# Optimization experiments

Measured on AMD Instinct MI355X. Metric: run time of the kernel, lower is better.

Reference implementation:

```python
import jax, jax.numpy as jnp
import numpy as np

SCALE_BASE = 512.0
GN_EPS = 1e-5


def _xpos(x, downscale):
    # x: [..., L, D]; XPOS rotary embedding with exponential length scale (torchscale)
    L, D = x.shape[-2], x.shape[-1]
    half = D // 2
    base = (jnp.arange(0, D, 2, dtype=jnp.float32) + 0.4 * D) / (1.4 * D)  # [half]
    min_pos = -(L // 2)
    power = (jnp.arange(min_pos, min_pos + L, dtype=jnp.float32) / SCALE_BASE)[:, None]
    scale = base[None, :] ** power  # [L, half]
    inv_freq = 1.0 / (10000.0 ** (jnp.arange(half, dtype=jnp.float32) / half))
    ang = jnp.arange(L, dtype=jnp.float32)[:, None] * inv_freq[None, :]  # [L, half]
    sin, cos = jnp.sin(ang), jnp.cos(ang)
    if downscale:
        scale = 1.0 / scale
    sin_s = jnp.repeat(sin * scale, 2, axis=-1)  # duplicate_interleave -> [L, D]
    cos_s = jnp.repeat(cos * scale, 2, axis=-1)
    x1, x2 = x[..., ::2], x[..., 1::2]
    rot = jnp.stack((-x2, x1), axis=-1).reshape(x.shape)  # rotate_every_two
    return x * cos_s + rot * sin_s


def _decay_mask(L, H):
    gammas = 1.0 - jnp.exp(jnp.linspace(np.log(1.0 / 32.0), np.log(1.0 / 512.0), H)).astype(jnp.float32)
    idx = jnp.arange(L)
    dist = idx[:, None] - idx[None, :]  # [L, L]
    causal = dist >= 0
    d = jnp.maximum(dist, 0).astype(jnp.float32)
    # gamma^|n-s| below diagonal, 0 above (gamma^inf = 0 in the torch version)
    return jnp.where(causal[None], gammas[:, None, None] ** d[None], 0.0)  # [H, L, L]


def setup_inputs() -> dict:
    key = jax.random.key(0)
    ks = jax.random.split(key, 9)
    B, L, D, H = 2, 2048, 1024, 16
    hd = D // H
    return {
        "query": jax.random.normal(ks[0], (B, L, D), jnp.float32),
        "key": jax.random.normal(ks[1], (B, L, D), jnp.float32),
        "value": jax.random.normal(ks[2], (B, L, D), jnp.float32),
        "W_Q": jax.random.normal(ks[3], (H, D, hd), jnp.float32) / D,
        "W_K": jax.random.normal(ks[4], (H, D, hd), jnp.float32) / D,
        "W_V": jax.random.normal(ks[5], (H, D, hd), jnp.float32) / D,
        "g_w": jax.random.normal(ks[6], (D, D), jnp.float32) * (2.0 / (D + D)) ** 0.5,
        "g_b": jnp.zeros((D,), jnp.float32),
        "out_w": jax.random.normal(ks[7], (D, D), jnp.float32) * (2.0 / (D + D)) ** 0.5,
        "out_b": jnp.zeros((D,), jnp.float32),
    }


def reference(query, key, value, W_Q, W_K, W_V, g_w, g_b, out_w, out_b):
    B, L, D = query.shape
    H = W_Q.shape[0]
    q = jnp.einsum('bld,hde->bhle', query, W_Q)
    k = jnp.einsum('bld,hde->bhle', key, W_K)
    v = jnp.einsum('bld,hde->bhle', value, W_V)
    q = _xpos(q, downscale=False)
    k = _xpos(k, downscale=True)
    # retention_parallel: QK^T * decay mask (no softmax, no scale), then @ V
    sim = jnp.einsum('bhnd,bhsd->bhns', q, k) * _decay_mask(L, H)[None]
    ret = jnp.einsum('bhns,bhsd->bhnd', sim, v)  # [B, H, L, hd]
    # GroupNorm(num_groups=H, affine=False) on (b n, h d): normalize per (b, h, n) over hd
    mu = ret.mean(axis=-1, keepdims=True)
    var = ret.var(axis=-1, keepdims=True)
    ret = (ret - mu) / jnp.sqrt(var + GN_EPS)
    ret = ret.transpose(0, 2, 1, 3).reshape(B, L, D)  # b h n d -> b n (h d)
    gate = jax.nn.silu(query @ g_w.T + g_b)
    return (ret * gate) @ out_w.T + out_b
```

## Files before the change

kernel.cpp:

```cpp
#include <hip/hip_runtime.h>
#include <cstdint>

#define B_  2
#define L_  2048
#define D_  1024
#define H_  16
#define HD_ 64
#define M_  (B_*L_)

#define MD  4194304u
#define DD  1048576u

#define OFF_XQB  0u
#define OFF_XKB  (MD)
#define OFF_XVB  (2u*MD)
#define OFF_WQT  (3u*MD)
#define OFF_WKT  (3u*MD + DD)
#define OFF_WVT  (3u*MD + 2u*DD)
#define OFF_GWB  (3u*MD + 3u*DD)
#define OFF_OWB  (3u*MD + 4u*DD)
#define OFF_GATE (3u*MD + 5u*DD)
#define OFF_QB2  (OFF_GATE + MD)
#define OFF_KB2  (OFF_QB2 + MD)
#define OFF_VTG  (OFF_KB2 + MD)
#define OFF_ABUF (OFF_VTG + MD)
#define OFF_F32  (OFF_ABUF + MD)

typedef __attribute__((ext_vector_type(8))) short bf16x8;
typedef __attribute__((ext_vector_type(4))) short s16x4;
typedef __attribute__((ext_vector_type(4))) float f32x4;

__device__ __forceinline__ unsigned short f2b(float x){
  union { float f; unsigned u; } a; a.f = x;
  unsigned r = a.u + 0x7FFFu + ((a.u >> 16) & 1u);
  return (unsigned short)(r >> 16);
}
__device__ __forceinline__ float b2f(unsigned short u){
  union { unsigned u; float f; } a; a.u = ((unsigned)u) << 16; return a.f;
}

__global__ __launch_bounds__(256) void prep_kernel(
    const float* __restrict__ q, const float* __restrict__ k,
    const float* __restrict__ v, const float* __restrict__ gw,
    const float* __restrict__ ow, const float* __restrict__ WQ,
    const float* __restrict__ WK, const float* __restrict__ WV,
    unsigned short* __restrict__ ws)
{
  __shared__ float t[32][33];
  const int bx = blockIdx.x, tid = threadIdx.x;
  if (bx < 14336) {
    size_t i = ((size_t)bx * 256 + tid) * 4;
    const float* src; unsigned short* dst;
    if (i < MD)            { src = q  + i;              dst = ws + OFF_XQB + i; }
    else if (i < 2u*MD)    { src = k  + (i - MD);       dst = ws + OFF_XKB + (i - MD); }
    else if (i < 3u*MD)    { src = v  + (i - 2u*MD);    dst = ws + OFF_XVB + (i - 2u*MD); }
    else if (i < 3u*MD+DD) { src = gw + (i - 3u*MD);    dst = ws + OFF_GWB + (i - 3u*MD); }
    else                   { src = ow + (i - 3u*MD-DD); dst = ws + OFF_OWB + (i - 3u*MD - DD); }
    float4 vv = *(const float4*)src;
    ushort4 o; o.x = f2b(vv.x); o.y = f2b(vv.y); o.z = f2b(vv.z); o.w = f2b(vv.w);
    *(ushort4*)dst = o;
  } else if (bx < 17408) {
    const int tb = bx - 14336;
    const int w = tb >> 10;
    const int tb2 = tb & 1023;
    const int h = tb2 >> 6, tt = tb2 & 63;
    const int e0 = (tt & 1) * 32, d0 = (tt >> 1) * 32;
    const float* in = (w == 0) ? WQ : (w == 1) ? WK : WV;
    unsigned short* out = ws + ((w == 0) ? OFF_WQT : (w == 1) ? OFF_WKT : OFF_WVT);
    const int x = tid & 31, y0 = tid >> 5;
    for (int yy = y0; yy < 32; yy += 8)
      t[yy][x] = in[((size_t)h * D_ + d0 + yy) * HD_ + e0 + x];
    __syncthreads();
    for (int yy = y0; yy < 32; yy += 8)
      out[((size_t)h * HD_ + e0 + yy) * D_ + d0 + x] = f2b(t[x][yy]);
  } else {
    float* fb = (float*)(ws + OFF_F32);
    const int idx = (bx - 17408) * 256 + tid;
    const int l = idx >> 5, i = idx & 31;
    const float base = (2.0f * (float)i + 0.4f * (float)HD_) / (1.4f * (float)HD_);
    const float p = (float)(l - L_ / 2) * (1.0f / 512.0f);
    const float sc = exp2f(p * log2f(base));
    const float invf = exp2f(-(float)i * (13.287712379549449f / 32.0f));
    float s, c; sincosf((float)l * invf, &s, &c);
    fb[          l * 32 + i] = c * sc;
    fb[ 65536 +  l * 32 + i] = s * sc;
    const float is = 1.0f / sc;
    fb[131072 +  l * 32 + i] = c * is;
    fb[196608 +  l * 32 + i] = s * is;
  }
}

__device__ __forceinline__ void gemm_body(
    const unsigned short* __restrict__ A, const unsigned short* __restrict__ Bt,
    float* __restrict__ outF, unsigned short* __restrict__ outB,
    const float* __restrict__ ct, const float* __restrict__ st,
    const float* __restrict__ bias, int mode, int ldc, int M0, int N0,
    char* As, char* Bs)
{
  const int tid = threadIdx.x;
  const int wave = tid >> 6, lane = tid & 63;
  const int wm = wave & 1, wn = wave >> 1;
  const int mlane = lane & 15, kgrp = lane >> 4;
  const int rl = lane >> 3, csel = lane & 7;
  const char* Ab = (const char*)A;
  const char* Bb = (const char*)Bt;

  f32x4 acc[4][2] = {};

  for (int K0 = 0; K0 < 1024; K0 += 64) {
    __syncthreads();
#pragma unroll
    for (int t = 0; t < 4; ++t) {
      const int row = wave * 32 + t * 8 + rl;
      const int gc = csel ^ (row & 7);
      const char* ga = Ab + ((size_t)(M0 + row) * 1024 + K0) * 2 + gc * 16;
      __builtin_amdgcn_global_load_lds(
          (const __attribute__((address_space(1))) void*)ga,
          (__attribute__((address_space(3))) void*)(As + (wave * 32 + t * 8) * 128 + lane * 16),
          16, 0, 0);
    }
#pragma unroll
    for (int t = 0; t < 2; ++t) {
      const int row = wave * 16 + t * 8 + rl;
      const int gc = csel ^ (row & 7);
      const char* gb = Bb + ((size_t)(N0 + row) * 1024 + K0) * 2 + gc * 16;
      __builtin_amdgcn_global_load_lds(
          (const __attribute__((address_space(1))) void*)gb,
          (__attribute__((address_space(3))) void*)(Bs + (wave * 16 + t * 8) * 128 + lane * 16),
          16, 0, 0);
    }
    __syncthreads();
#pragma unroll
    for (int kh = 0; kh < 2; ++kh) {
      bf16x8 af[4], bfr[2];
#pragma unroll
      for (int tm = 0; tm < 4; ++tm) {
        const int r = wm * 64 + tm * 16 + mlane;
        af[tm] = *(const bf16x8*)(As + r * 128 + (((kh * 4 + kgrp) ^ (r & 7)) << 4));
      }
#pragma unroll
      for (int tn = 0; tn < 2; ++tn) {
        const int r = wn * 32 + tn * 16 + mlane;
        bfr[tn] = *(const bf16x8*)(Bs + r * 128 + (((kh * 4 + kgrp) ^ (r & 7)) << 4));
      }
#pragma unroll
      for (int tm = 0; tm < 4; ++tm)
#pragma unroll
        for (int tn = 0; tn < 2; ++tn)
          acc[tm][tn] = __builtin_amdgcn_mfma_f32_16x16x32_bf16(af[tm], bfr[tn], acc[tm][tn], 0, 0, 0);
    }
  }

#pragma unroll
  for (int tm = 0; tm < 4; ++tm)
#pragma unroll
    for (int tn = 0; tn < 2; ++tn) {
      f32x4 v = acc[tm][tn];
#pragma unroll
      for (int r = 0; r < 4; ++r) {
        const int grow = M0 + wm * 64 + tm * 16 + (lane >> 4) * 4 + r;
        const int gcol = N0 + wn * 32 + tn * 16 + mlane;
        float val = v[r];
        if (mode == 1 || mode == 2) {
          const float partner = __shfl_xor(val, 1);
          const int l = grow & (L_ - 1);
          const int i = (gcol >> 1) & 31;
          const float c = ct[l * 32 + i], s = st[l * 32 + i];
          val = (gcol & 1) ? (val * c + partner * s) : (val * c - partner * s);
          outB[(size_t)grow * ldc + gcol] = f2b(val);
        } else if (mode == 0) {
          outB[(size_t)grow * ldc + gcol] = f2b(val);
        } else if (mode == 3) {
          const float x = val + bias[gcol];
          outB[(size_t)grow * ldc + gcol] = f2b(x / (1.0f + expf(-x)));
        } else {
          outF[(size_t)grow * ldc + gcol] = val + bias[gcol];
        }
      }
    }
}

__global__ __launch_bounds__(256) void gemm4_kernel(
    unsigned short* __restrict__ ws, const float* __restrict__ g_b)
{
  __shared__ __align__(16) char As[128 * 128];
  __shared__ __align__(16) char Bs[64 * 128];
  const int z = blockIdx.y, bx = blockIdx.x;
  float* fb = (float*)(ws + OFF_F32);
  const unsigned short *A, *Bt; unsigned short* outB;
  const float *ct = nullptr, *st = nullptr, *bias = nullptr;
  int mode, ldc, M0, N0;
  if (z == 0) {
    A = ws + OFF_XQB; Bt = ws + OFF_WQT; outB = ws + OFF_QB2;
    ct = fb; st = fb + 65536; mode = 1; ldc = D_;
    M0 = (bx & 31) * 128; N0 = (bx >> 5) * 64;
  } else if (z == 1) {
    A = ws + OFF_XKB; Bt = ws + OFF_WKT; outB = ws + OFF_KB2;
    ct = fb + 131072; st = fb + 196608; mode = 2; ldc = D_;
    M0 = (bx & 31) * 128; N0 = (bx >> 5) * 64;
  } else if (z == 2) {
    A = ws + OFF_WVT; Bt = ws + OFF_XVB; outB = ws + OFF_VTG;
    mode = 0; ldc = M_;
    M0 = (bx & 7) * 128; N0 = (bx >> 3) * 64;
  } else {
    A = ws + OFF_XQB; Bt = ws + OFF_GWB; outB = ws + OFF_GATE;
    bias = g_b; mode = 3; ldc = D_;
    M0 = (bx & 31) * 128; N0 = (bx >> 5) * 64;
  }
  gemm_body(A, Bt, nullptr, outB, ct, st, bias, mode, ldc, M0, N0, As, Bs);
}

__global__ __launch_bounds__(256) void gemm_final_kernel(
    unsigned short* __restrict__ ws, const float* __restrict__ out_b,
    float* __restrict__ out)
{
  __shared__ __align__(16) char As[128 * 128];
  __shared__ __align__(16) char Bs[64 * 128];
  gemm_body(ws + OFF_ABUF, ws + OFF_OWB, out, nullptr, nullptr, nullptr,
            out_b, 4, D_, blockIdx.x * 128, blockIdx.y * 64, As, Bs);
}

#define AQ_OFF 0
#define AK_OFF 8192
#define AV_OFF 16384
#define AP_OFF 24576

__global__ __launch_bounds__(256) void attn_mfma_kernel(
    const unsigned short* __restrict__ qg, const unsigned short* __restrict__ kg,
    const unsigned short* __restrict__ vtg, const unsigned short* __restrict__ gate,
    unsigned short* __restrict__ Abuf)
{
  __shared__ __align__(16) char smem[32768];
  const int tid = threadIdx.x, wave = tid >> 6, lane = tid & 63;
  const int mlane = lane & 15, kgrp = lane >> 4;
  const int rl = lane >> 3, csel = lane & 7;

  const int id = blockIdx.x;
  const int bh = id & 31, p = id >> 5;
  const int b = bh >> 4, h = bh & 15;

  const float lo   = -3.4657359027997265f;
  const float step = -0.1848392481493187f;
  const float gamma = 1.0f - expf(lo + (float)h * step);
  const float lg2g  = log2f(gamma);
  const float g1    = exp2f(-lg2g);
  const float gmr[4] = {1.0f, g1, g1 * g1, g1 * g1 * g1};

#pragma unroll 1
  for (int half = 0; half < 2; ++half) {
    const int xq = half ? (31 - p) : p;
    const int l0 = xq * 64;

    __syncthreads();
#pragma unroll
    for (int t = 0; t < 2; ++t) {
      const int row = 16 * wave + 8 * t + rl;
      const char* g = (const char*)(qg + (size_t)(b * L_ + l0 + row) * D_ + h * HD_ + ((csel ^ (row & 7)) << 3));
      __builtin_amdgcn_global_load_lds(
          (const __attribute__((address_space(1))) void*)g,
          (__attribute__((address_space(3))) void*)(smem + AQ_OFF + (16 * wave + 8 * t) * 128 + lane * 16),
          16, 0, 0);
    }
    __syncthreads();

    bf16x8 qa[2];
    {
      const int row = 16 * wave + mlane;
#pragma unroll
      for (int kk = 0; kk < 2; ++kk)
        qa[kk] = *(const bf16x8*)(smem + AQ_OFF + row * 128 + (((4 * kk + kgrp) ^ (row & 7)) << 4));
    }
    const float rqm = exp2f((float)(l0 + 16 * wave + mlane) * lg2g);

    f32x4 racc[4] = {};

    for (int it = 0; it <= xq; ++it) {
      const int s0 = it * 64;
      __syncthreads();
#pragma unroll
      for (int t = 0; t < 2; ++t) {
        const int row = 16 * wave + 8 * t + rl;
        const char* gk = (const char*)(kg + (size_t)(b * L_ + s0 + row) * D_ + h * HD_ + ((csel ^ (row & 7)) << 3));
        __builtin_amdgcn_global_load_lds(
            (const __attribute__((address_space(1))) void*)gk,
            (__attribute__((address_space(3))) void*)(smem + AK_OFF + (16 * wave + 8 * t) * 128 + lane * 16),
            16, 0, 0);
        const char* gv = (const char*)(vtg + (size_t)(h * HD_ + row) * M_ + b * L_ + s0 + ((csel ^ (row & 7)) << 3));
        __builtin_amdgcn_global_load_lds(
            (const __attribute__((address_space(1))) void*)gv,
            (__attribute__((address_space(3))) void*)(smem + AV_OFF + (16 * wave + 8 * t) * 128 + lane * 16),
            16, 0, 0);
      }
      __syncthreads();

      bf16x8 kb[4][2], vb[4][2];
#pragma unroll
      for (int tn = 0; tn < 4; ++tn)
#pragma unroll
        for (int kk = 0; kk < 2; ++kk) {
          const int row = 16 * tn + mlane;
          const int sw = ((4 * kk + kgrp) ^ (row & 7)) << 4;
          kb[tn][kk] = *(const bf16x8*)(smem + AK_OFF + row * 128 + sw);
          vb[tn][kk] = *(const bf16x8*)(smem + AV_OFF + row * 128 + sw);
        }
      float csb[4];
#pragma unroll
      for (int tn = 0; tn < 4; ++tn)
        csb[tn] = exp2f(-(float)(s0 + 16 * tn + 4 * kgrp) * lg2g);

      f32x4 sf[4];
#pragma unroll
      for (int tn = 0; tn < 4; ++tn) {
        f32x4 z = {};
        z = __builtin_amdgcn_mfma_f32_16x16x32_bf16(kb[tn][0], qa[0], z, 0, 0, 0);
        sf[tn] = __builtin_amdgcn_mfma_f32_16x16x32_bf16(kb[tn][1], qa[1], z, 0, 0, 0);
      }
      const int nrow = l0 + 16 * wave + mlane;
      const bool needMask = (it == xq);
      const int prow = 16 * wave + mlane;
#pragma unroll
      for (int tn = 0; tn < 4; ++tn) {
        const float wbase = rqm * csb[tn];
        const int sbase = s0 + 16 * tn + 4 * kgrp;
        float vv[4];
#pragma unroll
        for (int r = 0; r < 4; ++r) {
          float w = wbase * gmr[r];
          if (needMask) w = (nrow - (sbase + r) >= 0) ? w : 0.0f;
          vv[r] = sf[tn][r] * w;
        }
        s16x4 pk;
        pk[0] = (short)f2b(vv[0]); pk[1] = (short)f2b(vv[1]);
        pk[2] = (short)f2b(vv[2]); pk[3] = (short)f2b(vv[3]);
        *(s16x4*)(smem + AP_OFF + prow * 128 +
                  (((2 * tn + (kgrp >> 1)) ^ (prow & 7)) << 4) + ((kgrp & 1) << 3)) = pk;
      }
      __syncthreads();
      bf16x8 pa[2];
#pragma unroll
      for (int kk = 0; kk < 2; ++kk) {
        const int row = 16 * wave + mlane;
        pa[kk] = *(const bf16x8*)(smem + AP_OFF + row * 128 + (((4 * kk + kgrp) ^ (row & 7)) << 4));
      }
#pragma unroll
      for (int tn = 0; tn < 4; ++tn) {
        racc[tn] = __builtin_amdgcn_mfma_f32_16x16x32_bf16(pa[0], vb[tn][0], racc[tn], 0, 0, 0);
        racc[tn] = __builtin_amdgcn_mfma_f32_16x16x32_bf16(pa[1], vb[tn][1], racc[tn], 0, 0, 0);
      }
    }

#pragma unroll
    for (int r = 0; r < 4; ++r) {
      float vv[4], sm = 0.0f, sq = 0.0f;
#pragma unroll
      for (int tn = 0; tn < 4; ++tn) {
        vv[tn] = racc[tn][r];
        sm += vv[tn]; sq += vv[tn] * vv[tn];
      }
#pragma unroll
      for (int off = 1; off < 16; off <<= 1) {
        sm += __shfl_xor(sm, off);
        sq += __shfl_xor(sq, off);
      }
      const float mu = sm * (1.0f / 64.0f);
      float var = sq * (1.0f / 64.0f) - mu * mu;
      var = fmaxf(var, 0.0f);
      const float inv = rsqrtf(var + 1e-5f);
      const int row = l0 + 16 * wave + kgrp * 4 + r;
      const size_t base = (size_t)(b * L_ + row) * D_ + h * HD_;
#pragma unroll
      for (int tn = 0; tn < 4; ++tn) {
        const int c = 16 * tn + mlane;
        const float g = b2f(gate[base + c]);
        Abuf[base + c] = f2b((vv[tn] - mu) * inv * g);
      }
    }
  }
}

extern "C" void kernel_launch(void* const* d_in, const int* in_sizes, int n_in,
                              void* d_out, int out_size, void* d_ws, size_t ws_size,
                              hipStream_t stream)
{
  const float* query = (const float*)d_in[0];
  const float* key   = (const float*)d_in[1];
  const float* value = (const float*)d_in[2];
  const float* W_Q   = (const float*)d_in[3];
  const float* W_K   = (const float*)d_in[4];
  const float* W_V   = (const float*)d_in[5];
  const float* g_b   = (const float*)d_in[7];
  const float* out_b = (const float*)d_in[9];
  float* out = (float*)d_out;

  unsigned short* ws = (unsigned short*)d_ws;

  prep_kernel<<<17664, 256, 0, stream>>>(query, key, value,
                                         (const float*)d_in[6],
                                         (const float*)d_in[8],
                                         W_Q, W_K, W_V, ws);

  gemm4_kernel<<<dim3(512, 4), 256, 0, stream>>>(ws, g_b);

  attn_mfma_kernel<<<512, 256, 0, stream>>>(ws + OFF_QB2, ws + OFF_KB2,
                                            ws + OFF_VTG, ws + OFF_GATE,
                                            ws + OFF_ABUF);

  gemm_final_kernel<<<dim3(32, 16), 256, 0, stream>>>(ws, out_b, out);
}
```

Measured before the change: 236.0 us.

## Widen retention key tile to 128 and drop the P-tile block barrier

Result: no change. 235.2 us (-0.4%).

```diff
diff --git a/kernel.cpp b/kernel.cpp
--- a/kernel.cpp
+++ b/kernel.cpp
@@ -222,18 +222,19 @@
 
 #define AQ_OFF 0
 #define AK_OFF 8192
-#define AV_OFF 16384
-#define AP_OFF 24576
+#define AV_OFF 24576
+#define AP_OFF 40960
 
 __global__ __launch_bounds__(256) void attn_mfma_kernel(
     const unsigned short* __restrict__ qg, const unsigned short* __restrict__ kg,
     const unsigned short* __restrict__ vtg, const unsigned short* __restrict__ gate,
     unsigned short* __restrict__ Abuf)
 {
-  __shared__ __align__(16) char smem[32768];
+  __shared__ __align__(16) char smem[57344];
   const int tid = threadIdx.x, wave = tid >> 6, lane = tid & 63;
   const int mlane = lane & 15, kgrp = lane >> 4;
-  const int rl = lane >> 3, csel = lane & 7;
+  const int rl8 = lane >> 3, cs8 = lane & 7;
+  const int rl4 = lane >> 4, cs16 = lane & 15;
 
   const int id = blockIdx.x;
   const int bh = id & 31, p = id >> 5;
@@ -254,8 +255,8 @@
     __syncthreads();
 #pragma unroll
     for (int t = 0; t < 2; ++t) {
-      const int row = 16 * wave + 8 * t + rl;
-      const char* g = (const char*)(qg + (size_t)(b * L_ + l0 + row) * D_ + h * HD_ + ((csel ^ (row & 7)) << 3));
+      const int row = 16 * wave + 8 * t + rl8;
+      const char* g = (const char*)(qg + (size_t)(b * L_ + l0 + row) * D_ + h * HD_ + ((cs8 ^ (row & 7)) << 3));
       __builtin_amdgcn_global_load_lds(
           (const __attribute__((address_space(1))) void*)g,
           (__attribute__((address_space(3))) void*)(smem + AQ_OFF + (16 * wave + 8 * t) * 128 + lane * 16),
@@ -271,56 +272,51 @@
         qa[kk] = *(const bf16x8*)(smem + AQ_OFF + row * 128 + (((4 * kk + kgrp) ^ (row & 7)) << 4));
     }
     const float rqm = exp2f((float)(l0 + 16 * wave + mlane) * lg2g);
+    const int nrow = l0 + 16 * wave + mlane;
+    const int prow = 16 * wave + mlane;
 
     f32x4 racc[4] = {};
-
-    for (int it = 0; it <= xq; ++it) {
-      const int s0 = it * 64;
+    const int nst = (xq + 2) >> 1;
+
+    for (int it = 0; it < nst; ++it) {
+      const int s0 = it * 128;
       __syncthreads();
 #pragma unroll
-      for (int t = 0; t < 2; ++t) {
-        const int row = 16 * wave + 8 * t + rl;
-        const char* gk = (const char*)(kg + (size_t)(b * L_ + s0 + row) * D_ + h * HD_ + ((csel ^ (row & 7)) << 3));
+      for (int t = 0; t < 4; ++t) {
+        const int row = 32 * wave + 8 * t + rl8;
+        const char* gk = (const char*)(kg + (size_t)(b * L_ + s0 + row) * D_ + h * HD_ + ((cs8 ^ (row & 7)) << 3));
         __builtin_amdgcn_global_load_lds(
             (const __attribute__((address_space(1))) void*)gk,
-            (__attribute__((address_space(3))) void*)(smem + AK_OFF + (16 * wave + 8 * t) * 128 + lane * 16),
+            (__attribute__((address_space(3))) void*)(smem + AK_OFF + (32 * wave + 8 * t) * 128 + lane * 16),
             16, 0, 0);
-        const char* gv = (const char*)(vtg + (size_t)(h * HD_ + row) * M_ + b * L_ + s0 + ((csel ^ (row & 7)) << 3));
+      }
+#pragma unroll
+      for (int t = 0; t < 4; ++t) {
+        const int row = 16 * wave + 4 * t + rl4;
+        const char* gv = (const char*)(vtg + (size_t)(h * HD_ + row) * M_ + b * L_ + s0 + ((cs16 ^ (row & 7)) << 3));
         __builtin_amdgcn_global_load_lds(
             (const __attribute__((address_space(1))) void*)gv,
-            (__attribute__((address_space(3))) void*)(smem + AV_OFF + (16 * wave + 8 * t) * 128 + lane * 16),
+            (__attribute__((address_space(3))) void*)(smem + AV_OFF + (16 * wave + 4 * t) * 256 + lane * 16),
             16, 0, 0);
       }
       __syncthreads();
 
-      bf16x8 kb[4][2], vb[4][2];
-#pragma unroll
-      for (int tn = 0; tn < 4; ++tn)
-#pragma unroll
-        for (int kk = 0; kk < 2; ++kk) {
-          const int row = 16 * tn + mlane;
-          const int sw = ((4 * kk + kgrp) ^ (row & 7)) << 4;
-          kb[tn][kk] = *(const bf16x8*)(smem + AK_OFF + row * 128 + sw);
-          vb[tn][kk] = *(const bf16x8*)(smem + AV_OFF + row * 128 + sw);
-        }
-      float csb[4];
-#pragma unroll
-      for (int tn = 0; tn < 4; ++tn)
-        csb[tn] = exp2f(-(float)(s0 + 16 * tn + 4 * kgrp) * lg2g);
-
-      f32x4 sf[4];
-#pragma unroll
-      for (int tn = 0; tn < 4; ++tn) {
+      f32x4 sf[8];
+#pragma unroll
+      for (int tn = 0; tn < 8; ++tn) {
+        const int row = 16 * tn + mlane;
+        const bf16x8 kb0 = *(const bf16x8*)(smem + AK_OFF + row * 128 + ((kgrp ^ (row & 7)) << 4));
+        const bf16x8 kb1 = *(const bf16x8*)(smem + AK_OFF + row * 128 + (((4 + kgrp) ^ (row & 7)) << 4));
         f32x4 z = {};
-        z = __builtin_amdgcn_mfma_f32_16x16x32_bf16(kb[tn][0], qa[0], z, 0, 0, 0);
-        sf[tn] = __builtin_amdgcn_mfma_f32_16x16x32_bf16(kb[tn][1], qa[1], z, 0, 0, 0);
-      }
-      const int nrow = l0 + 16 * wave + mlane;
-      const bool needMask = (it == xq);
-      const int prow = 16 * wave + mlane;
-#pragma unroll
-      for (int tn = 0; tn < 4; ++tn) {
-        const float wbase = rqm * csb[tn];
+        z = __builtin_amdgcn_mfma_f32_16x16x32_bf16(kb0, qa[0], z, 0, 0, 0);
+        sf[tn] = __builtin_amdgcn_mfma_f32_16x16x32_bf16(kb1, qa[1], z, 0, 0, 0);
+      }
+
+      const bool needMask = (it == nst - 1);
+#pragma unroll
+      for (int tn = 0; tn < 8; ++tn) {
+        const float csb = exp2f(-(float)(s0 + 16 * tn + 4 * kgrp) * lg2g);
+        const float wbase = rqm * csb;
         const int sbase = s0 + 16 * tn + 4 * kgrp;
         float vv[4];
 #pragma unroll
@@ -332,20 +328,23 @@
         s16x4 pk;
         pk[0] = (short)f2b(vv[0]); pk[1] = (short)f2b(vv[1]);
         pk[2] = (short)f2b(vv[2]); pk[3] = (short)f2b(vv[3]);
-        *(s16x4*)(smem + AP_OFF + prow * 128 +
+        *(s16x4*)(smem + AP_OFF + prow * 256 +
                   (((2 * tn + (kgrp >> 1)) ^ (prow & 7)) << 4) + ((kgrp & 1) << 3)) = pk;
       }
-      __syncthreads();
-      bf16x8 pa[2];
-#pragma unroll
-      for (int kk = 0; kk < 2; ++kk) {
-        const int row = 16 * wave + mlane;
-        pa[kk] = *(const bf16x8*)(smem + AP_OFF + row * 128 + (((4 * kk + kgrp) ^ (row & 7)) << 4));
-      }
-#pragma unroll
-      for (int tn = 0; tn < 4; ++tn) {
-        racc[tn] = __builtin_amdgcn_mfma_f32_16x16x32_bf16(pa[0], vb[tn][0], racc[tn], 0, 0, 0);
-        racc[tn] = __builtin_amdgcn_mfma_f32_16x16x32_bf16(pa[1], vb[tn][1], racc[tn], 0, 0, 0);
+      asm volatile("s_waitcnt lgkmcnt(0)" ::: "memory");
+
+      bf16x8 pa[4];
+#pragma unroll
+      for (int kk = 0; kk < 4; ++kk)
+        pa[kk] = *(const bf16x8*)(smem + AP_OFF + prow * 256 + (((4 * kk + kgrp) ^ (prow & 7)) << 4));
+#pragma unroll
+      for (int te = 0; te < 4; ++te) {
+        const int rowE = 16 * te + mlane;
+#pragma unroll
+        for (int kk = 0; kk < 4; ++kk) {
+          const bf16x8 vbf = *(const bf16x8*)(smem + AV_OFF + rowE * 256 + (((4 * kk + kgrp) ^ (rowE & 7)) << 4));
+          racc[te] = __builtin_amdgcn_mfma_f32_16x16x32_bf16(pa[kk], vbf, racc[te], 0, 0, 0);
+        }
       }
     }
 
```
